# Kernel tuning notes

Hardware: AMD Instinct MI355X
Metric: run time of the kernel (lower is better)

Reference implementation:

```python
import jax, jax.numpy as jnp
import numpy as np

B, T = 4, 1024
L, D_IN = 3, 1024          # num HM-LSTM layers, per-layer hidden size
D = L * D_IN               # concatenated hidden size (3072)
EMB = 2048                 # shared embedding size
N_LIN = 2                  # linear_sizes = [2048, 2048]
OUT = 32000                # vocab
SCALE = 0.02


def setup_inputs() -> dict:
    key = jax.random.key(0)
    ks = jax.random.split(key, 8)
    return {
        "x": jax.random.normal(ks[0], (B, T, D), jnp.float32),
        "w": jax.random.normal(ks[1], (L, D), jnp.float32) * SCALE,        # gate weights, one [D] vector per layer
        "emb_w": jax.random.normal(ks[2], (L, D_IN, EMB), jnp.float32) * SCALE,
        "emb_b": jax.random.normal(ks[3], (L, EMB), jnp.float32) * SCALE,
        "lin_w": jax.random.normal(ks[4], (N_LIN, EMB, EMB), jnp.float32) * SCALE,
        "lin_b": jax.random.normal(ks[5], (N_LIN, EMB), jnp.float32) * SCALE,
        "out_w": jax.random.normal(ks[6], (EMB, OUT), jnp.float32) * SCALE,
        "out_b": jax.random.normal(ks[7], (OUT,), jnp.float32) * SCALE,
    }


def reference(x, w, emb_w, emb_b, lin_w, lin_b, out_w, out_b):
    Bx, Tx, Dx = x.shape
    # Per-layer scalar gates: sg_l = h @ w_l, g = sigmoid(sg)  -> [B, T, L]
    g = jax.nn.sigmoid(jnp.einsum('btd,ld->btl', x, w))
    # Split concatenated hidden into layers: [B, T, L, D_IN]
    xl = x.reshape(Bx, Tx, L, D_IN)
    # s = sum_l Linear_l(h_l * g_l); biases sum across layers
    s = jnp.einsum('btl,btli,lie->bte', g, xl, emb_w) + emb_b.sum(axis=0)
    h = jax.nn.relu(s)
    # fnn: stacked linears with tanh activation after each
    for i in range(lin_w.shape[0]):
        h = jnp.tanh(h @ lin_w[i] + lin_b[i])
    # final output projection
    return h @ out_w + out_b
```

## Files before the change

kernel.cpp:

```cpp
#include <hip/hip_runtime.h>
#include <math.h>

typedef __attribute__((ext_vector_type(8))) short short8;
typedef __attribute__((ext_vector_type(8))) unsigned short ushort8;
typedef __attribute__((ext_vector_type(4))) unsigned short ushort4v;
typedef __attribute__((ext_vector_type(4))) unsigned int uint4v;
typedef __attribute__((ext_vector_type(4))) float f32x4;

__device__ __forceinline__ unsigned short f2bf(float f) {
  union { float f; unsigned u; } v; v.f = f;
  unsigned u = v.u;
  return (unsigned short)((u + 0x7fffu + ((u >> 16) & 1u)) >> 16);
}

__device__ __forceinline__ void gload_lds16(const void* g, void* lds) {
  __builtin_amdgcn_global_load_lds(
      (const __attribute__((address_space(1))) unsigned int*)g,
      (__attribute__((address_space(3))) unsigned int*)lds, 16, 0, 0);
}

__global__ __launch_bounds__(256)
void gates_kernel(const float* __restrict__ x, const float* __restrict__ w,
                  unsigned short* __restrict__ xg) {
  const int n = blockIdx.x;
  const int t = threadIdx.x;
  const float* xr = x + (size_t)n * 3072;

  f32x4 xv[3];
#pragma unroll
  for (int c = 0; c < 3; ++c)
    xv[c] = *(const f32x4*)(xr + c * 1024 + t * 4);

  float p[3] = {0.f, 0.f, 0.f};
#pragma unroll
  for (int l = 0; l < 3; ++l) {
#pragma unroll
    for (int c = 0; c < 3; ++c) {
      f32x4 wv = *(const f32x4*)(w + l * 3072 + c * 1024 + t * 4);
      p[l] += xv[c][0] * wv[0] + xv[c][1] * wv[1] + xv[c][2] * wv[2] + xv[c][3] * wv[3];
    }
  }
#pragma unroll
  for (int off = 32; off; off >>= 1) {
    p[0] += __shfl_xor(p[0], off);
    p[1] += __shfl_xor(p[1], off);
    p[2] += __shfl_xor(p[2], off);
  }
  __shared__ float sred[4][3];
  const int wave = t >> 6, lane = t & 63;
  if (lane == 0) {
    sred[wave][0] = p[0]; sred[wave][1] = p[1]; sred[wave][2] = p[2];
  }
  __syncthreads();
  float g[3];
#pragma unroll
  for (int l = 0; l < 3; ++l) {
    float s = sred[0][l] + sred[1][l] + sred[2][l] + sred[3][l];
    g[l] = 1.f / (1.f + expf(-s));
  }
  unsigned short* orow = xg + (size_t)n * 3072;
#pragma unroll
  for (int c = 0; c < 3; ++c) {
    ushort4v o;
#pragma unroll
    for (int j = 0; j < 4; ++j) o[j] = f2bf(xv[c][j] * g[c]);
    *(ushort4v*)(orow + c * 1024 + t * 4) = o;
  }
}

__global__ __launch_bounds__(256)
void transcvt_kernel(const float* __restrict__ in, unsigned short* __restrict__ outp,
                     int R, int C) {
  __shared__ float tile[64][65];
  const int c0 = blockIdx.x * 64, r0 = blockIdx.y * 64;
  const int t = threadIdx.x;
  const int tr = t >> 4;
  const int tc = (t & 15) * 4;
#pragma unroll
  for (int p = 0; p < 4; ++p) {
    int r = p * 16 + tr;
    f32x4 v = *(const f32x4*)(in + (size_t)(r0 + r) * C + c0 + tc);
    tile[r][tc] = v[0]; tile[r][tc + 1] = v[1];
    tile[r][tc + 2] = v[2]; tile[r][tc + 3] = v[3];
  }
  __syncthreads();
  const int c = t >> 2;
  const int rb = (t & 3) * 16;
  ushort8 o0, o1;
#pragma unroll
  for (int j = 0; j < 8; ++j) o0[j] = f2bf(tile[rb + j][c]);
#pragma unroll
  for (int j = 0; j < 8; ++j) o1[j] = f2bf(tile[rb + 8 + j][c]);
  unsigned short* dst = outp + (size_t)(c0 + c) * R + r0 + rb;
  *(ushort8*)dst = o0;
  *(ushort8*)(dst + 8) = o1;
}

template <int EPI>
__global__ __launch_bounds__(256)
void gemm_tt(const unsigned short* __restrict__ A,
             const unsigned short* __restrict__ Bt,
             const float* __restrict__ bias,
             unsigned short* __restrict__ Cb,
             float* __restrict__ Cf,
             int K, int N) {
  __shared__ __align__(16) unsigned short As[128 * 64];
  __shared__ __align__(16) unsigned short Bs[128 * 64];

  const int tid = threadIdx.x;
  const int lane = tid & 63;
  const int wv = tid >> 6;
  const int wm = wv >> 1, wn = wv & 1;
  const int mt = blockIdx.x & 31;
  const int nt = blockIdx.x >> 5;
  const int m0 = mt * 128, n0 = nt * 128;
  const size_t strideB = (size_t)K * 2;

  f32x4 acc[4][4] = {};

  for (int kt = 0; kt < K; kt += 64) {
    __syncthreads();
#pragma unroll
    for (int i = 0; i < 4; ++i) {
      const int o = wv * 4096 + i * 1024 + lane * 16;
      const int row = o >> 7;
      const int sw = (((o >> 4) & 7) * 16) ^ ((row & 7) << 4);
      gload_lds16((const char*)A + (size_t)(m0 + row) * strideB + (size_t)kt * 2 + sw,
                  (char*)As + wv * 4096 + i * 1024);
      gload_lds16((const char*)Bt + (size_t)(n0 + row) * strideB + (size_t)kt * 2 + sw,
                  (char*)Bs + wv * 4096 + i * 1024);
    }
    __syncthreads();
#pragma unroll
    for (int kk = 0; kk < 2; ++kk) {
      short8 av[4], bv[4];
      const int kb = kk * 64 + (lane >> 4) * 16;
#pragma unroll
      for (int mi = 0; mi < 4; ++mi) {
        int row = wm * 64 + mi * 16 + (lane & 15);
        av[mi] = *(const short8*)((const char*)As + row * 128 + (kb ^ ((row & 7) << 4)));
      }
#pragma unroll
      for (int ni = 0; ni < 4; ++ni) {
        int row = wn * 64 + ni * 16 + (lane & 15);
        bv[ni] = *(const short8*)((const char*)Bs + row * 128 + (kb ^ ((row & 7) << 4)));
      }
#pragma unroll
      for (int mi = 0; mi < 4; ++mi)
#pragma unroll
        for (int ni = 0; ni < 4; ++ni)
          acc[mi][ni] = __builtin_amdgcn_mfma_f32_16x16x32_bf16(av[mi], bv[ni], acc[mi][ni], 0, 0, 0);
    }
  }

  const int lr = lane >> 4, lc = lane & 15;
#pragma unroll
  for (int ni = 0; ni < 4; ++ni) {
    int c = n0 + wn * 64 + ni * 16 + lc;
    float bb;
    if (EPI == 0) bb = bias[c] + bias[N + c] + bias[2 * N + c];
    else          bb = bias[c];
#pragma unroll
    for (int mi = 0; mi < 4; ++mi) {
      int r0 = m0 + wm * 64 + mi * 16 + lr * 4;
      f32x4 v = acc[mi][ni];
#pragma unroll
      for (int j = 0; j < 4; ++j) {
        float val = v[j] + bb;
        size_t idx = (size_t)(r0 + j) * N + c;
        if (EPI == 0) { val = val > 0.f ? val : 0.f; Cb[idx] = f2bf(val); }
        else if (EPI == 1) { Cb[idx] = f2bf(tanhf(val)); }
        else { Cf[idx] = val; }
      }
    }
  }
}

__global__ __launch_bounds__(512, 2)
void gemm8_out(const unsigned short* __restrict__ A,
               const unsigned short* __restrict__ Bt,
               const float* __restrict__ bias,
               float* __restrict__ Cf,
               int K, int N) {
  __shared__ __align__(16) unsigned short As8[2][256 * 64];
  __shared__ __align__(16) unsigned short Bs8[2][256 * 64];

  const int tid = threadIdx.x;
  const int lane = tid & 63;
  const int wid = tid >> 6;
  const int wm = wid >> 2, wn = wid & 3;

  const int bid = blockIdx.x;
  const int cpx = gridDim.x >> 3;
  const int lid = (bid & 7) * cpx + (bid >> 3);
  const int mt = lid & 15;
  const int ntile = lid >> 4;
  const int m0 = mt * 256, n0 = ntile * 256;
  const size_t strideB = (size_t)K * 2;
  const int kTiles = K >> 6;

  const unsigned short* smat = (wid < 4) ? A : Bt;
  char* sb = (wid < 4) ? (char*)As8 : (char*)Bs8;
  const int part = wid & 3;
  const int srow0 = ((wid < 4) ? m0 : n0) + part * 64 + (lane >> 3);
  const int ssw = ((lane & 7) ^ (lane >> 3)) << 4;

  auto stage8 = [&](int buf, int t) {
#pragma unroll
    for (int i = 0; i < 8; ++i)
      gload_lds16((const char*)smat + (size_t)(srow0 + i * 8) * strideB +
                      (size_t)t * 128 + ssw,
                  sb + buf * 32768 + part * 8192 + i * 1024);
  };

  const int l15 = lane & 15;
  const int kch = (lane >> 4) * 16;
  const int swr = (l15 & 7) << 4;

  f32x4 acc[8][4] = {};

  stage8(0, 0);
  stage8(1, 1);
  asm volatile("s_waitcnt vmcnt(8)" ::: "memory");
  __builtin_amdgcn_sched_barrier(0);
  __builtin_amdgcn_s_barrier();

  for (int t = 0; t < kTiles; ++t) {
    const char* ab = (const char*)As8 + (t & 1) * 32768;
    const char* bb = (const char*)Bs8 + (t & 1) * 32768;
    short8 av[4][2], bva[2][2], bvb[2][2];

#pragma unroll
    for (int mi = 0; mi < 4; ++mi)
#pragma unroll
      for (int ks = 0; ks < 2; ++ks) {
        int r = wm * 128 + mi * 16 + l15;
        av[mi][ks] = *(const short8*)(ab + r * 128 + ((ks * 64 + kch) ^ swr));
      }
#pragma unroll
    for (int ni = 0; ni < 2; ++ni)
#pragma unroll
      for (int ks = 0; ks < 2; ++ks) {
        int r = wn * 64 + ni * 16 + l15;
        bva[ni][ks] = *(const short8*)(bb + r * 128 + ((ks * 64 + kch) ^ swr));
      }
    __builtin_amdgcn_s_setprio(1);
#pragma unroll
    for (int ks = 0; ks < 2; ++ks)
#pragma unroll
      for (int mi = 0; mi < 4; ++mi)
#pragma unroll
        for (int ni = 0; ni < 2; ++ni)
          acc[mi][ni] = __builtin_amdgcn_mfma_f32_16x16x32_bf16(
              av[mi][ks], bva[ni][ks], acc[mi][ni], 0, 0, 0);
    __builtin_amdgcn_s_setprio(0);

#pragma unroll
    for (int ni = 0; ni < 2; ++ni)
#pragma unroll
      for (int ks = 0; ks < 2; ++ks) {
        int r = wn * 64 + 32 + ni * 16 + l15;
        bvb[ni][ks] = *(const short8*)(bb + r * 128 + ((ks * 64 + kch) ^ swr));
      }
    __builtin_amdgcn_s_setprio(1);
#pragma unroll
    for (int ks = 0; ks < 2; ++ks)
#pragma unroll
      for (int mi = 0; mi < 4; ++mi)
#pragma unroll
        for (int ni = 0; ni < 2; ++ni)
          acc[mi][2 + ni] = __builtin_amdgcn_mfma_f32_16x16x32_bf16(
              av[mi][ks], bvb[ni][ks], acc[mi][2 + ni], 0, 0, 0);
    __builtin_amdgcn_s_setprio(0);

#pragma unroll
    for (int mi = 0; mi < 4; ++mi)
#pragma unroll
      for (int ks = 0; ks < 2; ++ks) {
        int r = wm * 128 + 64 + mi * 16 + l15;
        av[mi][ks] = *(const short8*)(ab + r * 128 + ((ks * 64 + kch) ^ swr));
      }
    __builtin_amdgcn_s_setprio(1);
#pragma unroll
    for (int ks = 0; ks < 2; ++ks)
#pragma unroll
      for (int mi = 0; mi < 4; ++mi)
#pragma unroll
        for (int ni = 0; ni < 2; ++ni)
          acc[4 + mi][2 + ni] = __builtin_amdgcn_mfma_f32_16x16x32_bf16(
              av[mi][ks], bvb[ni][ks], acc[4 + mi][2 + ni], 0, 0, 0);
    __builtin_amdgcn_s_setprio(0);

    __builtin_amdgcn_s_setprio(1);
#pragma unroll
    for (int ks = 0; ks < 2; ++ks)
#pragma unroll
      for (int mi = 0; mi < 4; ++mi)
#pragma unroll
        for (int ni = 0; ni < 2; ++ni)
          acc[4 + mi][ni] = __builtin_amdgcn_mfma_f32_16x16x32_bf16(
              av[mi][ks], bva[ni][ks], acc[4 + mi][ni], 0, 0, 0);
    __builtin_amdgcn_s_setprio(0);

    if (t + 1 < kTiles) {
      __builtin_amdgcn_sched_barrier(0);
      __builtin_amdgcn_s_barrier();
      if (t + 2 < kTiles) {
        stage8(t & 1, t + 2);
        asm volatile("s_waitcnt vmcnt(8)" ::: "memory");
      } else {
        asm volatile("s_waitcnt vmcnt(0)" ::: "memory");
      }
      __builtin_amdgcn_sched_barrier(0);
      __builtin_amdgcn_s_barrier();
    }
  }

  const int lr = lane >> 4;
#pragma unroll
  for (int ni = 0; ni < 4; ++ni) {
    int c = n0 + wn * 64 + ni * 16 + l15;
    float bb2 = bias[c];
#pragma unroll
    for (int mi = 0; mi < 8; ++mi) {
      int r0 = m0 + wm * 128 + mi * 16 + lr * 4;
#pragma unroll
      for (int j = 0; j < 4; ++j)
        Cf[(size_t)(r0 + j) * N + c] = acc[mi][ni][j] + bb2;
    }
  }
}

template <int EPI>
__global__ __launch_bounds__(256)
void gemm_bf16(const unsigned short* __restrict__ A,
               const float* __restrict__ B,
               const float* __restrict__ bias,
               unsigned short* __restrict__ Cb,
               float* __restrict__ Cf,
               int K, int N) {
  __shared__ __align__(16) unsigned short As[128 * 64];
  __shared__ __align__(16) unsigned short Bs[128 * 64];

  const int tid = threadIdx.x;
  const int lane = tid & 63;
  const int wv = tid >> 6;
  const int wm = wv >> 1, wn = wv & 1;
  const int mt = blockIdx.x & 31;
  const int nt = blockIdx.x >> 5;
  const int m0 = mt * 128, n0 = nt * 128;

  f32x4 acc[4][4] = {};

  for (int kt = 0; kt < K; kt += 64) {
    __syncthreads();
#pragma unroll
    for (int i = 0; i < 4; ++i) {
      int q = tid + 256 * i;
      int row = q >> 3;
      int kc = q & 7;
      uint4v v = *(const uint4v*)((const char*)A +
                   ((size_t)(m0 + row) * K + kt) * 2 + kc * 16);
      *(uint4v*)((char*)As + row * 128 + ((kc * 16) ^ ((row & 7) << 4))) = v;
    }
#pragma unroll
    for (int gi = 0; gi < 4; ++gi) {
      int q = tid + 256 * gi;
      int nn = q & 127;
      int k8 = q >> 7;
      const float* src = B + (size_t)(kt + k8 * 8) * N + (n0 + nn);
      ushort8 tv;
#pragma unroll
      for (int j = 0; j < 8; ++j) tv[j] = f2bf(src[(size_t)j * N]);
      *(ushort8*)((char*)Bs + nn * 128 + ((k8 * 16) ^ ((nn & 7) << 4))) = tv;
    }
    __syncthreads();
#pragma unroll
    for (int kk = 0; kk < 2; ++kk) {
      short8 av[4], bv[4];
      const int kb = kk * 64 + (lane >> 4) * 16;
#pragma unroll
      for (int mi = 0; mi < 4; ++mi) {
        int row = wm * 64 + mi * 16 + (lane & 15);
        av[mi] = *(const short8*)((const char*)As + row * 128 + (kb ^ ((row & 7) << 4)));
      }
#pragma unroll
      for (int ni = 0; ni < 4; ++ni) {
        int row = wn * 64 + ni * 16 + (lane & 15);
        bv[ni] = *(const short8*)((const char*)Bs + row * 128 + (kb ^ ((row & 7) << 4)));
      }
#pragma unroll
      for (int mi = 0; mi < 4; ++mi)
#pragma unroll
        for (int ni = 0; ni < 4; ++ni)
          acc[mi][ni] = __builtin_amdgcn_mfma_f32_16x16x32_bf16(av[mi], bv[ni], acc[mi][ni], 0, 0, 0);
    }
  }

  const int lr = lane >> 4, lc = lane & 15;
#pragma unroll
  for (int ni = 0; ni < 4; ++ni) {
    int c = n0 + wn * 64 + ni * 16 + lc;
    float bb = bias[c];
#pragma unroll
    for (int mi = 0; mi < 4; ++mi) {
      int r0 = m0 + wm * 64 + mi * 16 + lr * 4;
      f32x4 v = acc[mi][ni];
#pragma unroll
      for (int j = 0; j < 4; ++j) {
        float val = v[j] + bb;
        size_t idx = (size_t)(r0 + j) * N + c;
        if (EPI == 1) { Cb[idx] = f2bf(tanhf(val)); }
        else { Cf[idx] = val; }
      }
    }
  }
}

extern "C" void kernel_launch(void* const* d_in, const int* in_sizes, int n_in,
                              void* d_out, int out_size, void* d_ws, size_t ws_size,
                              hipStream_t stream) {
  const float* x     = (const float*)d_in[0];
  const float* w     = (const float*)d_in[1];
  const float* emb_w = (const float*)d_in[2];
  const float* emb_b = (const float*)d_in[3];
  const float* lin_w = (const float*)d_in[4];
  const float* lin_b = (const float*)d_in[5];
  const float* out_w = (const float*)d_in[6];
  const float* out_b = (const float*)d_in[7];
  float* out = (float*)d_out;

  char* ob = (char*)d_out;
  unsigned short* xg      = (unsigned short*)ob;
  unsigned short* h0      = (unsigned short*)(ob + (((size_t)128) << 20));
  unsigned short* h1      = (unsigned short*)(ob + (((size_t)160) << 20));
  unsigned short* emb_wT  = (unsigned short*)(ob + (((size_t)192) << 20));
  unsigned short* lin_wT0 = (unsigned short*)(ob + (((size_t)208) << 20));
  unsigned short* lin_wT1 = (unsigned short*)(ob + (((size_t)224) << 20));
  unsigned short* h2      = (unsigned short*)d_ws;
  unsigned short* out_wT  = (unsigned short*)((char*)d_ws + (((size_t)32) << 20));
  const bool fast4 = ws_size >= ((((size_t)32) << 20) + (size_t)32000 * 2048 * 2);

  gates_kernel<<<4096, 256, 0, stream>>>(x, w, xg);
  transcvt_kernel<<<dim3(32, 48), 256, 0, stream>>>(emb_w, emb_wT, 3072, 2048);
  transcvt_kernel<<<dim3(32, 32), 256, 0, stream>>>(lin_w, lin_wT0, 2048, 2048);
  transcvt_kernel<<<dim3(32, 32), 256, 0, stream>>>(lin_w + 2048 * 2048, lin_wT1, 2048, 2048);
  if (fast4)
    transcvt_kernel<<<dim3(500, 32), 256, 0, stream>>>(out_w, out_wT, 2048, 32000);

  gemm_tt<0><<<32 * 16, 256, 0, stream>>>(xg, emb_wT, emb_b, h0, nullptr, 3072, 2048);
  gemm_tt<1><<<32 * 16, 256, 0, stream>>>(h0, lin_wT0, lin_b, h1, nullptr, 2048, 2048);
  gemm_tt<1><<<32 * 16, 256, 0, stream>>>(h1, lin_wT1, lin_b + 2048, h2, nullptr, 2048, 2048);
  if (fast4)
    gemm8_out<<<16 * 125, 512, 0, stream>>>(h2, out_wT, out_b, out, 2048, 32000);
  else
    gemm_bf16<2><<<32 * 250, 256, 0, stream>>>(h2, out_w, out_b, nullptr, out, 2048, 32000);
}
```

Before: 956.8 us.

## Interleave quarter-tile global-to-LDS loads with MFMA phases in output GEMM

Splits the per-tile LDS staging into four half-matrix chunks (A/B halves) issued between the four MFMA phases, with barriers after each phase, replacing the single bulk stage8 at the end of each k-iteration. Some halves of the next tile and the tile after are prefetched into buffers as soon as the region being overwritten has been read. The goal is to spread memory traffic across compute and avoid the serialized load burst per iteration, at the cost of many more workgroup barriers and tighter buffer-reuse ordering that must be correct.

```diff
diff --git a/kernel.cpp b/kernel.cpp
--- a/kernel.cpp
+++ b/kernel.cpp
@@ -18,6 +18,10 @@
       (const __attribute__((address_space(1))) unsigned int*)g,
       (__attribute__((address_space(3))) unsigned int*)lds, 16, 0, 0);
 }
+
+#define SBAR() do { __builtin_amdgcn_sched_barrier(0); \
+                    __builtin_amdgcn_s_barrier();      \
+                    __builtin_amdgcn_sched_barrier(0); } while (0)
 
 __global__ __launch_bounds__(256)
 void gates_kernel(const float* __restrict__ x, const float* __restrict__ w,
@@ -199,18 +203,25 @@
   const size_t strideB = (size_t)K * 2;
   const int kTiles = K >> 6;
 
-  const unsigned short* smat = (wid < 4) ? A : Bt;
-  char* sb = (wid < 4) ? (char*)As8 : (char*)Bs8;
-  const int part = wid & 3;
-  const int srow0 = ((wid < 4) ? m0 : n0) + part * 64 + (lane >> 3);
   const int ssw = ((lane & 7) ^ (lane >> 3)) << 4;
-
-  auto stage8 = [&](int buf, int t) {
-#pragma unroll
-    for (int i = 0; i < 8; ++i)
-      gload_lds16((const char*)smat + (size_t)(srow0 + i * 8) * strideB +
+  const int srow = lane >> 3;
+  const int sdst = wid * 1024;
+
+  auto stageA = [&](int half, int buf, int t) {
+#pragma unroll
+    for (int j = 0; j < 2; ++j)
+      gload_lds16((const char*)A +
+                      (size_t)(m0 + half * 128 + j * 64 + wid * 8 + srow) * strideB +
                       (size_t)t * 128 + ssw,
-                  sb + buf * 32768 + part * 8192 + i * 1024);
+                  (char*)As8 + buf * 32768 + half * 16384 + j * 8192 + sdst);
+  };
+  auto stageB = [&](int half, int buf, int t) {
+#pragma unroll
+    for (int j = 0; j < 2; ++j)
+      gload_lds16((const char*)Bt +
+                      (size_t)(n0 + half * 128 + j * 64 + wid * 8 + srow) * strideB +
+                      (size_t)t * 128 + ssw,
+                  (char*)Bs8 + buf * 32768 + half * 16384 + j * 8192 + sdst);
   };
 
   const int l15 = lane & 15;
@@ -219,15 +230,17 @@
 
   f32x4 acc[8][4] = {};
 
-  stage8(0, 0);
-  stage8(1, 1);
-  asm volatile("s_waitcnt vmcnt(8)" ::: "memory");
-  __builtin_amdgcn_sched_barrier(0);
-  __builtin_amdgcn_s_barrier();
-
-  for (int t = 0; t < kTiles; ++t) {
-    const char* ab = (const char*)As8 + (t & 1) * 32768;
-    const char* bb = (const char*)Bs8 + (t & 1) * 32768;
+  stageA(0, 0, 0); stageA(1, 0, 0); stageB(0, 0, 0); stageB(1, 0, 0);
+  stageB(0, 1, 1); stageA(0, 1, 1);
+  asm volatile("s_waitcnt vmcnt(4)" ::: "memory");
+  SBAR();
+
+  for (int u = 0; u < kTiles; ++u) {
+    const int cur = u & 1;
+    const char* ab = (const char*)As8 + cur * 32768;
+    const char* bb = (const char*)Bs8 + cur * 32768;
+    const bool st12 = (u + 1 < kTiles);
+    const bool st34 = (u + 2 < kTiles);
     short8 av[4][2], bva[2][2], bvb[2][2];
 
 #pragma unroll
@@ -244,6 +257,8 @@
         int r = wn * 64 + ni * 16 + l15;
         bva[ni][ks] = *(const short8*)(bb + r * 128 + ((ks * 64 + kch) ^ swr));
       }
+    if (st12) stageA(1, cur ^ 1, u + 1);
+    SBAR();
     __builtin_amdgcn_s_setprio(1);
 #pragma unroll
     for (int ks = 0; ks < 2; ++ks)
@@ -254,6 +269,7 @@
           acc[mi][ni] = __builtin_amdgcn_mfma_f32_16x16x32_bf16(
               av[mi][ks], bva[ni][ks], acc[mi][ni], 0, 0, 0);
     __builtin_amdgcn_s_setprio(0);
+    SBAR();
 
 #pragma unroll
     for (int ni = 0; ni < 2; ++ni)
@@ -262,6 +278,8 @@
         int r = wn * 64 + 32 + ni * 16 + l15;
         bvb[ni][ks] = *(const short8*)(bb + r * 128 + ((ks * 64 + kch) ^ swr));
       }
+    if (st12) stageB(1, cur ^ 1, u + 1);
+    SBAR();
     __builtin_amdgcn_s_setprio(1);
 #pragma unroll
     for (int ks = 0; ks < 2; ++ks)
@@ -272,6 +290,7 @@
           acc[mi][2 + ni] = __builtin_amdgcn_mfma_f32_16x16x32_bf16(
               av[mi][ks], bvb[ni][ks], acc[mi][2 + ni], 0, 0, 0);
     __builtin_amdgcn_s_setprio(0);
+    SBAR();
 
 #pragma unroll
     for (int mi = 0; mi < 4; ++mi)
@@ -280,6 +299,8 @@
         int r = wm * 128 + 64 + mi * 16 + l15;
         av[mi][ks] = *(const short8*)(ab + r * 128 + ((ks * 64 + kch) ^ swr));
       }
+    if (st34) stageB(0, cur, u + 2);
+    SBAR();
     __builtin_amdgcn_s_setprio(1);
 #pragma unroll
     for (int ks = 0; ks < 2; ++ks)
@@ -290,7 +311,10 @@
           acc[4 + mi][2 + ni] = __builtin_amdgcn_mfma_f32_16x16x32_bf16(
               av[mi][ks], bvb[ni][ks], acc[4 + mi][2 + ni], 0, 0, 0);
     __builtin_amdgcn_s_setprio(0);
-
+    SBAR();
+
+    if (st34) stageA(0, cur, u + 2);
+    SBAR();
     __builtin_amdgcn_s_setprio(1);
 #pragma unroll
     for (int ks = 0; ks < 2; ++ks)
@@ -301,19 +325,9 @@
           acc[4 + mi][ni] = __builtin_amdgcn_mfma_f32_16x16x32_bf16(
               av[mi][ks], bva[ni][ks], acc[4 + mi][ni], 0, 0, 0);
     __builtin_amdgcn_s_setprio(0);
-
-    if (t + 1 < kTiles) {
-      __builtin_amdgcn_sched_barrier(0);
-      __builtin_amdgcn_s_barrier();
-      if (t + 2 < kTiles) {
-        stage8(t & 1, t + 2);
-        asm volatile("s_waitcnt vmcnt(8)" ::: "memory");
-      } else {
-        asm volatile("s_waitcnt vmcnt(0)" ::: "memory");
-      }
-      __builtin_amdgcn_sched_barrier(0);
-      __builtin_amdgcn_s_barrier();
-    }
+    if (st34) { asm volatile("s_waitcnt vmcnt(4)" ::: "memory"); }
+    else      { asm volatile("s_waitcnt vmcnt(0)" ::: "memory"); }
+    SBAR();
   }
 
   const int lr = lane >> 4;
```

Result: slower. 978.0 us (+2.2%).
